# Optimization experiments

Measured on AMD Instinct MI355X. Metric: run time of the kernel, lower is better.

Reference implementation:

```python
import jax, jax.numpy as jnp
import numpy as np

B, S, D, H = 1, 2048, 1024, 16
HD = D // H
THRESHOLD_PCT = 0.95
SPARSITY = 0.9
TOPK = max(1, int(S * (1.0 - SPARSITY)))  # 204


def setup_inputs() -> dict:
    key = jax.random.key(0)
    ks = jax.random.split(key, 6)
    inp = {
        'x': jax.random.normal(ks[0], (B, S, D), dtype=jnp.float32),
        'Wq': jax.random.normal(ks[1], (D, D), dtype=jnp.float32) * 0.02,
        'bq': jnp.zeros((D,), jnp.float32),
        'Wk': jax.random.normal(ks[2], (D, D), dtype=jnp.float32) * 0.02,
        'bk': jnp.zeros((D,), jnp.float32),
        'Wv': jax.random.normal(ks[3], (D, D), dtype=jnp.float32) * 0.02,
        'bv': jnp.zeros((D,), jnp.float32),
        'Wo': jax.random.normal(ks[4], (D, D), dtype=jnp.float32) * 0.02,
        'bo': jnp.zeros((D,), jnp.float32),
    }
    return inp


def _heads(t):  # [B,S,D] -> [B,H,S,HD]
    return t.reshape(B, S, H, HD).transpose(0, 2, 1, 3)


def reference(x, Wq, bq, Wk, bk, Wv, bv, Wo, bo):
    q = _heads(x @ Wq + bq)
    k = _heads(x @ Wk + bk)
    v = _heads(x @ Wv + bv)
    scores = jnp.einsum('bhqd,bhkd->bhqk', q, k) / jnp.sqrt(jnp.float32(HD))

    # --- dynamic threshold mask (per batch,head quantile over all S*S scores) ---
    flat = scores.reshape(B, H, S * S)
    thr = jnp.quantile(flat, THRESHOLD_PCT, axis=-1)[..., None, None]  # [B,H,1,1]
    thresh_mask = scores >= thr
    # fallback: if kept fraction exceeds (1 - sparsity_ratio), use per-row top-k
    cond = jnp.mean(thresh_mask.astype(scores.dtype)) > (1.0 - SPARSITY)
    kth = jax.lax.top_k(scores, TOPK)[0][..., -1:]  # k-th largest per row
    topk_mask = scores >= kth
    mask = jnp.where(cond, topk_mask, thresh_mask)

    masked = jnp.where(mask, scores, -jnp.inf)
    attn = jax.nn.softmax(masked, axis=-1)
    out = jnp.einsum('bhqk,bhkd->bhqd', attn, v)
    out = out.transpose(0, 2, 1, 3).reshape(B, S, D)
    return out @ Wo + bo
```

## Files before the change

kernel.cpp:

```cpp
#include <hip/hip_runtime.h>
#include <math.h>

#define SS 2048
#define DD 1024
#define HH 16
#define CAPC 49152u
#define LCAP 2048

#define K_A 3984587u
#define K_B 3984588u
#define QFRAC 0.85f
#define WSCALE 2048.0f
#define WSCALE_INV (1.0f/2048.0f)
#define ESHIFT 4.0f

typedef _Float16 f16x8 __attribute__((ext_vector_type(8)));
typedef _Float16 f16x4 __attribute__((ext_vector_type(4)));
typedef float    f32x4 __attribute__((ext_vector_type(4)));

__device__ __forceinline__ unsigned sortkey(float f) {
  unsigned b = __float_as_uint(f);
  return (b & 0x80000000u) ? ~b : (b | 0x80000000u);
}
__device__ __forceinline__ float inv_sortkey(unsigned u) {
  unsigned b = (u & 0x80000000u) ? (u ^ 0x80000000u) : ~u;
  return __uint_as_float(b);
}

__global__ __launch_bounds__(256) void split_x(const float* __restrict__ x,
                                               _Float16* __restrict__ xh,
                                               _Float16* __restrict__ xl)
{
  const int i = blockIdx.x * 256 + threadIdx.x;
  float4 v = ((const float4*)x)[i];
  float vv[4] = {v.x, v.y, v.z, v.w};
  f16x4 h, l;
#pragma unroll
  for (int j = 0; j < 4; ++j) {
    _Float16 hh = (_Float16)vv[j];
    h[j] = hh;
    l[j] = (_Float16)(vv[j] - (float)hh);
  }
  ((f16x4*)xh)[i] = h;
  ((f16x4*)xl)[i] = l;
}

__global__ __launch_bounds__(256) void split_wT(const float* __restrict__ Wq,
                                                const float* __restrict__ Wk,
                                                const float* __restrict__ Wv,
                                                const float* __restrict__ Wo,
                                                _Float16* __restrict__ wplanes)
{
  const int z = blockIdx.z;
  const float* W = (z == 0) ? Wq : (z == 1) ? Wk : (z == 2) ? Wv : Wo;
  _Float16* WhT = wplanes + (size_t)(2*z)     * (1024*1024);
  _Float16* WlT = wplanes + (size_t)(2*z + 1) * (1024*1024);
  __shared__ float tile[64][65];
  const int t  = threadIdx.x;
  const int r  = t >> 2;
  const int c0 = (t & 3) * 16;
  const int k0 = blockIdx.y * 64;
  const int n0 = blockIdx.x * 64;
#pragma unroll
  for (int j = 0; j < 4; ++j) {
    float4 v = *(const float4*)&W[(size_t)(k0 + r) * 1024 + n0 + c0 + j*4];
    tile[r][c0+j*4+0] = v.x; tile[r][c0+j*4+1] = v.y;
    tile[r][c0+j*4+2] = v.z; tile[r][c0+j*4+3] = v.w;
  }
  __syncthreads();
  f16x8 h0, h1, l0, l1;
#pragma unroll
  for (int j = 0; j < 8; ++j) {
    float v = tile[c0 + j][r] * WSCALE;
    _Float16 h = (_Float16)v;
    h0[j] = h; l0[j] = (_Float16)(v - (float)h);
  }
#pragma unroll
  for (int j = 0; j < 8; ++j) {
    float v = tile[c0 + 8 + j][r] * WSCALE;
    _Float16 h = (_Float16)v;
    h1[j] = h; l1[j] = (_Float16)(v - (float)h);
  }
  const size_t o = (size_t)(n0 + r) * 1024 + k0 + c0;
  *(f16x8*)&WhT[o]     = h0;
  *(f16x8*)&WhT[o + 8] = h1;
  *(f16x8*)&WlT[o]     = l0;
  *(f16x8*)&WlT[o + 8] = l1;
}

__device__ __forceinline__ void gemm_mfma_body(const _Float16* __restrict__ Ah,
                                               const _Float16* __restrict__ Al,
                                               const _Float16* __restrict__ BhT,
                                               const _Float16* __restrict__ BlT,
                                               const float* __restrict__ bias,
                                               _Float16* __restrict__ Oh,
                                               _Float16* __restrict__ Ol,
                                               float* __restrict__ Of,
                                               int mode, int bm, int bn)
{
  const int wave = threadIdx.x >> 6, lane = threadIdx.x & 63;
  const int wr = wave >> 1, wc = wave & 1;
  const int m0 = bm * 128 + wr * 64;
  const int n0 = bn * 128 + wc * 64;
  const int lr = lane & 15;
  const int ko = lane >> 4;

  f32x4 acc[4][4];
#pragma unroll
  for (int i = 0; i < 4; ++i)
#pragma unroll
    for (int j = 0; j < 4; ++j) acc[i][j] = (f32x4){0.f, 0.f, 0.f, 0.f};

  for (int kk = 0; kk < 32; ++kk) {
    const int kof = kk*32 + ko*8;
    f16x8 aH[4], aL[4], bH[4], bL[4];
#pragma unroll
    for (int i = 0; i < 4; ++i) {
      const size_t aoff = (size_t)(m0 + i*16 + lr) * 1024 + kof;
      aH[i] = *(const f16x8*)(Ah + aoff);
      aL[i] = *(const f16x8*)(Al + aoff);
      const size_t boff = (size_t)(n0 + i*16 + lr) * 1024 + kof;
      bH[i] = *(const f16x8*)(BhT + boff);
      bL[i] = *(const f16x8*)(BlT + boff);
    }
#pragma unroll
    for (int i = 0; i < 4; ++i)
#pragma unroll
      for (int j = 0; j < 4; ++j) {
        acc[i][j] = __builtin_amdgcn_mfma_f32_16x16x32_f16(aL[i], bL[j], acc[i][j], 0, 0, 0);
        acc[i][j] = __builtin_amdgcn_mfma_f32_16x16x32_f16(aH[i], bL[j], acc[i][j], 0, 0, 0);
        acc[i][j] = __builtin_amdgcn_mfma_f32_16x16x32_f16(aL[i], bH[j], acc[i][j], 0, 0, 0);
        acc[i][j] = __builtin_amdgcn_mfma_f32_16x16x32_f16(aH[i], bH[j], acc[i][j], 0, 0, 0);
      }
  }

#pragma unroll
  for (int i = 0; i < 4; ++i) {
#pragma unroll
    for (int j = 0; j < 4; ++j) {
      if (mode == 2) {
        const int col  = n0 + j*16 + lr;
        const int row0 = m0 + i*16 + ko*4;
        f16x4 hv, lv;
#pragma unroll
        for (int r = 0; r < 4; ++r) {
          const float val = acc[i][j][r] * WSCALE_INV + bias[col];
          _Float16 h = (_Float16)val;
          hv[r] = h; lv[r] = (_Float16)(val - (float)h);
        }
        *(f16x4*)&Oh[(size_t)col * 2048 + row0] = hv;
        *(f16x4*)&Ol[(size_t)col * 2048 + row0] = lv;
      } else {
#pragma unroll
        for (int r = 0; r < 4; ++r) {
          const int row = m0 + i*16 + ko*4 + r;
          const int col = n0 + j*16 + lr;
          const float val = acc[i][j][r] * WSCALE_INV + bias[col];
          if (mode == 1) {
            Of[(size_t)row * 1024 + col] = val;
          } else {
            _Float16 h = (_Float16)val;
            Oh[(size_t)row * 1024 + col] = h;
            Ol[(size_t)row * 1024 + col] = (_Float16)(val - (float)h);
          }
        }
      }
    }
  }
}

__global__ __launch_bounds__(256) void gemm_mfma_qkv(const _Float16* __restrict__ xh,
                                                     const _Float16* __restrict__ xl,
                                                     const _Float16* __restrict__ wplanes,
                                                     const float* __restrict__ bq,
                                                     const float* __restrict__ bk,
                                                     const float* __restrict__ bv,
                                                     _Float16* __restrict__ Qh,
                                                     _Float16* __restrict__ Ql,
                                                     _Float16* __restrict__ Kh,
                                                     _Float16* __restrict__ Kl,
                                                     _Float16* __restrict__ VtH,
                                                     _Float16* __restrict__ VtL)
{
  const int z = blockIdx.z;
  const _Float16* BhT = wplanes + (size_t)(2*z)     * (1024*1024);
  const _Float16* BlT = wplanes + (size_t)(2*z + 1) * (1024*1024);
  const float* bias = (z == 0) ? bq : (z == 1) ? bk : bv;
  _Float16* Oh = (z == 0) ? Qh : (z == 1) ? Kh : VtH;
  _Float16* Ol = (z == 0) ? Ql : (z == 1) ? Kl : VtL;
  gemm_mfma_body(xh, xl, BhT, BlT, bias, Oh, Ol, nullptr, (z == 2) ? 2 : 0,
                 blockIdx.y, blockIdx.x);
}

__global__ __launch_bounds__(256) void gemm_mfma_o(const _Float16* __restrict__ ctxh,
                                                   const _Float16* __restrict__ ctxl,
                                                   const _Float16* __restrict__ wplanes,
                                                   const float* __restrict__ bo,
                                                   float* __restrict__ out)
{
  gemm_mfma_body(ctxh, ctxl,
                 wplanes + (size_t)6 * (1024*1024),
                 wplanes + (size_t)7 * (1024*1024),
                 bo, nullptr, nullptr, out, 1, blockIdx.y, blockIdx.x);
}

__global__ __launch_bounds__(512) void scores_hist(const _Float16* __restrict__ Qh,
                                                   const _Float16* __restrict__ Ql,
                                                   const _Float16* __restrict__ Kh,
                                                   const _Float16* __restrict__ Kl,
                                                   unsigned* __restrict__ ghist)
{
  const int bn = blockIdx.x, bm = blockIdx.y, h = blockIdx.z;
  const int wave = threadIdx.x >> 6, lane = threadIdx.x & 63;
  const int wr = wave >> 1, wc = wave & 1;
  const int m0 = bm * 256 + wr * 64;
  const int n0 = bn * 128 + wc * 64;
  const int lr = lane & 15;
  const int ko = lane >> 4;

  __shared__ unsigned lh[16384];
  for (int i = threadIdx.x; i < 16384; i += 512) lh[i] = 0;
  __syncthreads();

  f32x4 acc[4][4];
#pragma unroll
  for (int i = 0; i < 4; ++i)
#pragma unroll
    for (int j = 0; j < 4; ++j) acc[i][j] = (f32x4){0.f, 0.f, 0.f, 0.f};

#pragma unroll
  for (int kk = 0; kk < 2; ++kk) {
    f16x8 aH[4], aL[4], bH[4], bL[4];
#pragma unroll
    for (int i = 0; i < 4; ++i) {
      const size_t aoff = (size_t)(m0 + i*16 + lr) * 1024 + h*64 + kk*32 + ko*8;
      aH[i] = *(const f16x8*)(Qh + aoff);
      aL[i] = *(const f16x8*)(Ql + aoff);
      const size_t boff = (size_t)(n0 + i*16 + lr) * 1024 + h*64 + kk*32 + ko*8;
      bH[i] = *(const f16x8*)(Kh + boff);
      bL[i] = *(const f16x8*)(Kl + boff);
    }
#pragma unroll
    for (int i = 0; i < 4; ++i)
#pragma unroll
      for (int j = 0; j < 4; ++j) {
        acc[i][j] = __builtin_amdgcn_mfma_f32_16x16x32_f16(aL[i], bL[j], acc[i][j], 0, 0, 0);
        acc[i][j] = __builtin_amdgcn_mfma_f32_16x16x32_f16(aH[i], bL[j], acc[i][j], 0, 0, 0);
        acc[i][j] = __builtin_amdgcn_mfma_f32_16x16x32_f16(aL[i], bH[j], acc[i][j], 0, 0, 0);
        acc[i][j] = __builtin_amdgcn_mfma_f32_16x16x32_f16(aH[i], bH[j], acc[i][j], 0, 0, 0);
      }
  }

#pragma unroll
  for (int i = 0; i < 4; ++i)
#pragma unroll
    for (int j = 0; j < 4; ++j)
#pragma unroll
      for (int r = 0; r < 4; ++r) {
        const float val = acc[i][j][r] * 0.125f;
        atomicAdd(&lh[sortkey(val) >> 18], 1u);
      }
  __syncthreads();
  unsigned* __restrict__ gh = ghist + (size_t)h * 16384;
  for (int i = threadIdx.x; i < 16384; i += 512) {
    const unsigned c = lh[i];
    if (c) atomicAdd(&gh[i], c);
  }
}

__global__ __launch_bounds__(256) void init14(unsigned* __restrict__ ghist,
                                              unsigned* __restrict__ ccnt)
{
  int i = blockIdx.x * 256 + threadIdx.x;
  for (; i < HH * 16384; i += gridDim.x * 256) ghist[i] = 0;
  if (blockIdx.x == 0 && threadIdx.x < HH) ccnt[threadIdx.x] = 0;
}

__global__ __launch_bounds__(256) void scan14(const unsigned* __restrict__ ghist,
                                              unsigned* __restrict__ state)
{
  const int hh = blockIdx.x;
  const int t = threadIdx.x;
  __shared__ unsigned part[256];
  __shared__ unsigned out[4];
  const unsigned* __restrict__ hb = ghist + (size_t)hh * 16384;
  unsigned s = 0;
  for (int j = 0; j < 64; ++j) s += hb[t*64 + j];
  part[t] = s;
  __syncthreads();
  if (t == 0) {
    unsigned run = 0;
    for (int i = 0; i < 256; ++i) { unsigned tmp = part[i]; part[i] = run; run += tmp; }
  }
  __syncthreads();
  const unsigned cum0 = part[t];
  if (K_A >= cum0 && K_A < cum0 + s) {
    unsigned c2 = cum0;
    for (int j = 0; j < 64; ++j) {
      const unsigned c = hb[t*64 + j];
      if (K_A < c2 + c) {
        const unsigned binA = t*64 + j;
        const unsigned residA = K_A - c2;
        unsigned binB, residB;
        if (residA + 1 < c) { binB = binA; residB = residA + 1; }
        else {
          unsigned bb = binA + 1;
          while (bb < 16384 && hb[bb] == 0) ++bb;
          if (bb >= 16384) bb = 16383;
          binB = bb; residB = 0;
        }
        out[0] = binA; out[1] = residA; out[2] = binB; out[3] = residB;
        break;
      }
      c2 += c;
    }
  }
  __syncthreads();
  if (t < 4) state[hh*4 + t] = out[t];
}

__global__ __launch_bounds__(512) void compact_recompute(const _Float16* __restrict__ Qh,
                                                         const _Float16* __restrict__ Ql,
                                                         const _Float16* __restrict__ Kh,
                                                         const _Float16* __restrict__ Kl,
                                                         const unsigned* __restrict__ state,
                                                         unsigned* __restrict__ cand,
                                                         unsigned* __restrict__ ccnt)
{
  const int bn = blockIdx.x, bm = blockIdx.y, h = blockIdx.z;
  const int wave = threadIdx.x >> 6, lane = threadIdx.x & 63;
  const int wr = wave >> 1, wc = wave & 1;
  const int m0 = bm * 256 + wr * 64;
  const int n0 = bn * 128 + wc * 64;
  const int lr = lane & 15;
  const int ko = lane >> 4;

  __shared__ unsigned lbuf[LCAP];
  __shared__ unsigned lcnt, gbase;
  if (threadIdx.x == 0) lcnt = 0;
  __syncthreads();
  const unsigned binA = state[h*4+0];
  const unsigned binB = state[h*4+2];
  unsigned* __restrict__ mycand = cand + (size_t)h * CAPC;

  f32x4 acc[4][4];
#pragma unroll
  for (int i = 0; i < 4; ++i)
#pragma unroll
    for (int j = 0; j < 4; ++j) acc[i][j] = (f32x4){0.f, 0.f, 0.f, 0.f};

#pragma unroll
  for (int kk = 0; kk < 2; ++kk) {
    f16x8 aH[4], aL[4], bH[4], bL[4];
#pragma unroll
    for (int i = 0; i < 4; ++i) {
      const size_t aoff = (size_t)(m0 + i*16 + lr) * 1024 + h*64 + kk*32 + ko*8;
      aH[i] = *(const f16x8*)(Qh + aoff);
      aL[i] = *(const f16x8*)(Ql + aoff);
      const size_t boff = (size_t)(n0 + i*16 + lr) * 1024 + h*64 + kk*32 + ko*8;
      bH[i] = *(const f16x8*)(Kh + boff);
      bL[i] = *(const f16x8*)(Kl + boff);
    }
#pragma unroll
    for (int i = 0; i < 4; ++i)
#pragma unroll
      for (int j = 0; j < 4; ++j) {
        acc[i][j] = __builtin_amdgcn_mfma_f32_16x16x32_f16(aL[i], bL[j], acc[i][j], 0, 0, 0);
        acc[i][j] = __builtin_amdgcn_mfma_f32_16x16x32_f16(aH[i], bL[j], acc[i][j], 0, 0, 0);
        acc[i][j] = __builtin_amdgcn_mfma_f32_16x16x32_f16(aL[i], bH[j], acc[i][j], 0, 0, 0);
        acc[i][j] = __builtin_amdgcn_mfma_f32_16x16x32_f16(aH[i], bH[j], acc[i][j], 0, 0, 0);
      }
  }

#pragma unroll
  for (int i = 0; i < 4; ++i)
#pragma unroll
    for (int j = 0; j < 4; ++j)
#pragma unroll
      for (int r = 0; r < 4; ++r) {
        const float val = acc[i][j][r] * 0.125f;
        const unsigned u = sortkey(val);
        const unsigned bin = u >> 18;
        if (bin == binA || bin == binB) {
          unsigned id = atomicAdd(&lcnt, 1u);
          if (id < LCAP) lbuf[id] = u;
          else { unsigned g = atomicAdd(&ccnt[h], 1u); if (g < CAPC) mycand[g] = u; }
        }
      }
  __syncthreads();
  const unsigned n = (lcnt < LCAP) ? lcnt : LCAP;
  if (threadIdx.x == 0) gbase = n ? atomicAdd(&ccnt[h], n) : 0u;
  __syncthreads();
  const unsigned gb = gbase;
  for (unsigned i = threadIdx.x; i < n; i += 512)
    if (gb + i < CAPC) mycand[gb + i] = lbuf[i];
}

__global__ __launch_bounds__(256) void final_select_list(const unsigned* __restrict__ cand,
                                                         const unsigned* __restrict__ ccnt,
                                                         const unsigned* __restrict__ state,
                                                         float* __restrict__ thr)
{
  const int hh = blockIdx.x;
  const int t = threadIdx.x;
  __shared__ unsigned hist[256];
  __shared__ unsigned digitS, kresS;
  __shared__ float valS[2];
  unsigned n = ccnt[hh]; if (n > CAPC) n = CAPC;
  const unsigned* __restrict__ list = cand + (size_t)hh * CAPC;
  for (int tgt = 0; tgt < 2; ++tgt) {
    unsigned pfx = state[hh*4 + tgt*2];
    unsigned k   = state[hh*4 + tgt*2 + 1];
    for (int r = 0; r < 3; ++r) {
      const int s = (r == 0) ? 10 : (r == 1) ? 2 : 0;
      const int w = (r == 2) ? 2 : 8;
      const unsigned nb = 1u << w;
      hist[t] = 0;
      __syncthreads();
      for (unsigned i = t; i < n; i += 256) {
        const unsigned u = list[i];
        if ((u >> (s + w)) == pfx) atomicAdd(&hist[(u >> s) & (nb - 1)], 1u);
      }
      __syncthreads();
      if (t == 0) {
        unsigned cum = 0, b = 0;
        for (; b < nb; ++b) { const unsigned c = hist[b]; if (cum + c > k) break; cum += c; }
        if (b == nb) b = nb - 1;
        digitS = b; kresS = k - cum;
      }
      __syncthreads();
      pfx = (pfx << w) | digitS;
      k = kresS;
    }
    if (t == 0) valS[tgt] = inv_sortkey(pfx);
    __syncthreads();
  }
  if (t == 0) thr[hh] = valS[0] + QFRAC * (valS[1] - valS[0]);
}

__global__ __launch_bounds__(256) void flash_pv(const _Float16* __restrict__ Qh,
                                                const _Float16* __restrict__ Ql,
                                                const _Float16* __restrict__ Kh,
                                                const _Float16* __restrict__ Kl,
                                                const _Float16* __restrict__ VtH,
                                                const _Float16* __restrict__ VtL,
                                                const float* __restrict__ thrArr,
                                                _Float16* __restrict__ ctxh,
                                                _Float16* __restrict__ ctxl)
{
  const int bm = blockIdx.x;
  const int h  = blockIdx.y;
  const int wave = threadIdx.x >> 6, lane = threadIdx.x & 63;
  const int lr = lane & 15;
  const int ko = lane >> 4;
  const int m0 = bm * 64;
  const float thr = thrArr[h];

  __shared__ _Float16 Plds[64][136];
  __shared__ float rsLDS[64][4];

  f16x8 qH[4][2], qL[4][2];
#pragma unroll
  for (int i = 0; i < 4; ++i)
#pragma unroll
    for (int kk = 0; kk < 2; ++kk) {
      const size_t aoff = (size_t)(m0 + i*16 + lr) * 1024 + h*64 + kk*32 + ko*8;
      qH[i][kk] = *(const f16x8*)(Qh + aoff);
      qL[i][kk] = *(const f16x8*)(Ql + aoff);
    }

  f32x4 oacc[4];
#pragma unroll
  for (int i = 0; i < 4; ++i) oacc[i] = (f32x4){0.f, 0.f, 0.f, 0.f};
  float rs[4][4];
#pragma unroll
  for (int i = 0; i < 4; ++i)
#pragma unroll
    for (int r = 0; r < 4; ++r) rs[i][r] = 0.f;

  const int d0 = wave * 16;

  for (int kt = 0; kt < 16; ++kt) {
    const int n0 = kt*128 + wave*32;
    f32x4 sacc[4][2];
#pragma unroll
    for (int i = 0; i < 4; ++i)
#pragma unroll
      for (int j = 0; j < 2; ++j) sacc[i][j] = (f32x4){0.f, 0.f, 0.f, 0.f};

#pragma unroll
    for (int kk = 0; kk < 2; ++kk) {
      f16x8 bH[2], bL[2];
#pragma unroll
      for (int j = 0; j < 2; ++j) {
        const size_t boff = (size_t)(n0 + j*16 + lr) * 1024 + h*64 + kk*32 + ko*8;
        bH[j] = *(const f16x8*)(Kh + boff);
        bL[j] = *(const f16x8*)(Kl + boff);
      }
#pragma unroll
      for (int i = 0; i < 4; ++i)
#pragma unroll
        for (int j = 0; j < 2; ++j) {
          sacc[i][j] = __builtin_amdgcn_mfma_f32_16x16x32_f16(qL[i][kk], bL[j], sacc[i][j], 0, 0, 0);
          sacc[i][j] = __builtin_amdgcn_mfma_f32_16x16x32_f16(qH[i][kk], bL[j], sacc[i][j], 0, 0, 0);
          sacc[i][j] = __builtin_amdgcn_mfma_f32_16x16x32_f16(qL[i][kk], bH[j], sacc[i][j], 0, 0, 0);
          sacc[i][j] = __builtin_amdgcn_mfma_f32_16x16x32_f16(qH[i][kk], bH[j], sacc[i][j], 0, 0, 0);
        }
    }

#pragma unroll
    for (int i = 0; i < 4; ++i)
#pragma unroll
      for (int j = 0; j < 2; ++j)
#pragma unroll
        for (int r = 0; r < 4; ++r) {
          const float val = sacc[i][j][r] * 0.125f;
          const float p = (val >= thr) ? __expf(val - thr - ESHIFT) : 0.f;
          rs[i][r] += p;
          Plds[i*16 + ko*4 + r][wave*32 + j*16 + lr] = (_Float16)p;
        }
    __syncthreads();

#pragma unroll
    for (int kk2 = 0; kk2 < 4; ++kk2) {
      f16x8 pa[4];
#pragma unroll
      for (int i = 0; i < 4; ++i)
        pa[i] = *(const f16x8*)&Plds[i*16 + lr][kk2*32 + ko*8];
      const size_t vo = (size_t)(h*64 + d0 + lr) * 2048 + kt*128 + kk2*32 + ko*8;
      const f16x8 vH = *(const f16x8*)(VtH + vo);
      const f16x8 vL = *(const f16x8*)(VtL + vo);
#pragma unroll
      for (int i = 0; i < 4; ++i) {
        oacc[i] = __builtin_amdgcn_mfma_f32_16x16x32_f16(pa[i], vL, oacc[i], 0, 0, 0);
        oacc[i] = __builtin_amdgcn_mfma_f32_16x16x32_f16(pa[i], vH, oacc[i], 0, 0, 0);
      }
    }
    __syncthreads();
  }

#pragma unroll
  for (int i = 0; i < 4; ++i)
#pragma unroll
    for (int r = 0; r < 4; ++r) {
      float v = rs[i][r];
      v += __shfl_xor(v, 1); v += __shfl_xor(v, 2);
      v += __shfl_xor(v, 4); v += __shfl_xor(v, 8);
      rs[i][r] = v;
    }
  if (lr == 0) {
#pragma unroll
    for (int i = 0; i < 4; ++i)
#pragma unroll
      for (int r = 0; r < 4; ++r)
        rsLDS[i*16 + ko*4 + r][wave] = rs[i][r];
  }
  __syncthreads();

#pragma unroll
  for (int i = 0; i < 4; ++i)
#pragma unroll
    for (int r = 0; r < 4; ++r) {
      const int lrow = i*16 + ko*4 + r;
      const float tot = rsLDS[lrow][0] + rsLDS[lrow][1] + rsLDS[lrow][2] + rsLDS[lrow][3];
      const float val = oacc[i][r] / tot;
      const size_t oidx = (size_t)(m0 + lrow) * 1024 + h*64 + d0 + lr;
      _Float16 hv = (_Float16)val;
      ctxh[oidx] = hv;
      ctxl[oidx] = (_Float16)(val - (float)hv);
    }
}

extern "C" void kernel_launch(void* const* d_in, const int* in_sizes, int n_in,
                              void* d_out, int out_size, void* d_ws, size_t ws_size,
                              hipStream_t stream)
{
  const float* x  = (const float*)d_in[0];
  const float* Wq = (const float*)d_in[1];
  const float* bq = (const float*)d_in[2];
  const float* Wk = (const float*)d_in[3];
  const float* bk = (const float*)d_in[4];
  const float* Wv = (const float*)d_in[5];
  const float* bv = (const float*)d_in[6];
  const float* Wo = (const float*)d_in[7];
  const float* bo = (const float*)d_in[8];
  float* out = (float*)d_out;
  char*  ws  = (char*)d_ws;

  const size_t MB = 1u << 20;
  _Float16* xh      = (_Float16*)(ws + 0*MB);
  _Float16* xl      = (_Float16*)(ws + 4*MB);
  _Float16* wplanes = (_Float16*)(ws + 8*MB);
  _Float16* Qh      = (_Float16*)(ws + 24*MB);
  _Float16* Ql      = (_Float16*)(ws + 28*MB);
  _Float16* Kh      = (_Float16*)(ws + 32*MB);
  _Float16* Kl      = (_Float16*)(ws + 36*MB);
  _Float16* VtH     = (_Float16*)(ws + 40*MB);
  _Float16* VtL     = (_Float16*)(ws + 44*MB);
  _Float16* ctxh    = (_Float16*)(ws + 48*MB);
  _Float16* ctxl    = (_Float16*)(ws + 52*MB);
  const size_t base = 56*MB;
  unsigned* state = (unsigned*)(ws + base);
  float*    thr   = (float*)(ws + base + 4096);
  unsigned* ccnt  = (unsigned*)(ws + base + 8192);
  unsigned* ghist = (unsigned*)(ws + base + 16384);
  unsigned* cand  = (unsigned*)(ws + base + 16384 + 1048576);

  split_x<<<2048, 256, 0, stream>>>(x, xh, xl);
  split_wT<<<dim3(16, 16, 4), 256, 0, stream>>>(Wq, Wk, Wv, Wo, wplanes);
  gemm_mfma_qkv<<<dim3(8, 16, 3), 256, 0, stream>>>(xh, xl, wplanes, bq, bk, bv,
                                                    Qh, Ql, Kh, Kl, VtH, VtL);

  init14<<<256, 256, 0, stream>>>(ghist, ccnt);
  scores_hist<<<dim3(16, 8, HH), 512, 0, stream>>>(Qh, Ql, Kh, Kl, ghist);
  scan14<<<HH, 256, 0, stream>>>(ghist, state);
  compact_recompute<<<dim3(16, 8, HH), 512, 0, stream>>>(Qh, Ql, Kh, Kl, state, cand, ccnt);
  final_select_list<<<HH, 256, 0, stream>>>(cand, ccnt, state, thr);
  flash_pv<<<dim3(32, HH), 256, 0, stream>>>(Qh, Ql, Kh, Kl, VtH, VtL, thr, ctxh, ctxl);

  gemm_mfma_o<<<dim3(8, 16), 256, 0, stream>>>(ctxh, ctxl, wplanes, bo, out);
}
```

Before: 601.1 us.

## Split GEMM tiles across 8 waves with register prefetch, halve flash_pv rows

The QKV and output GEMMs now run 512-thread blocks, with each of 8 waves owning a 64x32 sub-tile instead of 64x64. The K-loop loads the next k-slice of A and B fragments into registers while the MFMAs for the current slice run. flash_pv handles 32 query rows per block instead of 64 and launches twice as many blocks. The aim is more waves in flight and latency hiding on the global loads, at the cost of more redundant K/V loads in flash_pv and more A-fragment reloads across waves in the GEMMs.

```diff
diff --git a/kernel.cpp b/kernel.cpp
--- a/kernel.cpp
+++ b/kernel.cpp
@@ -99,45 +99,73 @@
                                                int mode, int bm, int bn)
 {
   const int wave = threadIdx.x >> 6, lane = threadIdx.x & 63;
-  const int wr = wave >> 1, wc = wave & 1;
+  const int wr = wave >> 2, wc = wave & 3;
   const int m0 = bm * 128 + wr * 64;
-  const int n0 = bn * 128 + wc * 64;
+  const int n0 = bn * 128 + wc * 32;
   const int lr = lane & 15;
   const int ko = lane >> 4;
 
-  f32x4 acc[4][4];
+  f32x4 acc[4][2];
 #pragma unroll
   for (int i = 0; i < 4; ++i)
 #pragma unroll
-    for (int j = 0; j < 4; ++j) acc[i][j] = (f32x4){0.f, 0.f, 0.f, 0.f};
-
-  for (int kk = 0; kk < 32; ++kk) {
-    const int kof = kk*32 + ko*8;
-    f16x8 aH[4], aL[4], bH[4], bL[4];
+    for (int j = 0; j < 2; ++j) acc[i][j] = (f32x4){0.f, 0.f, 0.f, 0.f};
+
+  f16x8 aH[4], aL[4], bH[2], bL[2];
+  {
+    const int kof = ko*8;
 #pragma unroll
     for (int i = 0; i < 4; ++i) {
       const size_t aoff = (size_t)(m0 + i*16 + lr) * 1024 + kof;
       aH[i] = *(const f16x8*)(Ah + aoff);
       aL[i] = *(const f16x8*)(Al + aoff);
-      const size_t boff = (size_t)(n0 + i*16 + lr) * 1024 + kof;
-      bH[i] = *(const f16x8*)(BhT + boff);
-      bL[i] = *(const f16x8*)(BlT + boff);
+    }
+#pragma unroll
+    for (int j = 0; j < 2; ++j) {
+      const size_t boff = (size_t)(n0 + j*16 + lr) * 1024 + kof;
+      bH[j] = *(const f16x8*)(BhT + boff);
+      bL[j] = *(const f16x8*)(BlT + boff);
+    }
+  }
+
+  for (int kk = 0; kk < 32; ++kk) {
+    f16x8 nAH[4], nAL[4], nBH[2], nBL[2];
+    if (kk < 31) {
+      const int kof = (kk+1)*32 + ko*8;
+#pragma unroll
+      for (int i = 0; i < 4; ++i) {
+        const size_t aoff = (size_t)(m0 + i*16 + lr) * 1024 + kof;
+        nAH[i] = *(const f16x8*)(Ah + aoff);
+        nAL[i] = *(const f16x8*)(Al + aoff);
+      }
+#pragma unroll
+      for (int j = 0; j < 2; ++j) {
+        const size_t boff = (size_t)(n0 + j*16 + lr) * 1024 + kof;
+        nBH[j] = *(const f16x8*)(BhT + boff);
+        nBL[j] = *(const f16x8*)(BlT + boff);
+      }
     }
 #pragma unroll
     for (int i = 0; i < 4; ++i)
 #pragma unroll
-      for (int j = 0; j < 4; ++j) {
+      for (int j = 0; j < 2; ++j) {
         acc[i][j] = __builtin_amdgcn_mfma_f32_16x16x32_f16(aL[i], bL[j], acc[i][j], 0, 0, 0);
         acc[i][j] = __builtin_amdgcn_mfma_f32_16x16x32_f16(aH[i], bL[j], acc[i][j], 0, 0, 0);
         acc[i][j] = __builtin_amdgcn_mfma_f32_16x16x32_f16(aL[i], bH[j], acc[i][j], 0, 0, 0);
         acc[i][j] = __builtin_amdgcn_mfma_f32_16x16x32_f16(aH[i], bH[j], acc[i][j], 0, 0, 0);
       }
+    if (kk < 31) {
+#pragma unroll
+      for (int i = 0; i < 4; ++i) { aH[i] = nAH[i]; aL[i] = nAL[i]; }
+#pragma unroll
+      for (int j = 0; j < 2; ++j) { bH[j] = nBH[j]; bL[j] = nBL[j]; }
+    }
   }
 
 #pragma unroll
   for (int i = 0; i < 4; ++i) {
 #pragma unroll
-    for (int j = 0; j < 4; ++j) {
+    for (int j = 0; j < 2; ++j) {
       if (mode == 2) {
         const int col  = n0 + j*16 + lr;
         const int row0 = m0 + i*16 + ko*4;
@@ -169,7 +197,7 @@
   }
 }
 
-__global__ __launch_bounds__(256) void gemm_mfma_qkv(const _Float16* __restrict__ xh,
+__global__ __launch_bounds__(512) void gemm_mfma_qkv(const _Float16* __restrict__ xh,
                                                      const _Float16* __restrict__ xl,
                                                      const _Float16* __restrict__ wplanes,
                                                      const float* __restrict__ bq,
@@ -192,7 +220,7 @@
                  blockIdx.y, blockIdx.x);
 }
 
-__global__ __launch_bounds__(256) void gemm_mfma_o(const _Float16* __restrict__ ctxh,
+__global__ __launch_bounds__(512) void gemm_mfma_o(const _Float16* __restrict__ ctxh,
                                                    const _Float16* __restrict__ ctxl,
                                                    const _Float16* __restrict__ wplanes,
                                                    const float* __restrict__ bo,
@@ -453,15 +481,15 @@
   const int wave = threadIdx.x >> 6, lane = threadIdx.x & 63;
   const int lr = lane & 15;
   const int ko = lane >> 4;
-  const int m0 = bm * 64;
+  const int m0 = bm * 32;
   const float thr = thrArr[h];
 
-  __shared__ _Float16 Plds[64][136];
-  __shared__ float rsLDS[64][4];
-
-  f16x8 qH[4][2], qL[4][2];
-#pragma unroll
-  for (int i = 0; i < 4; ++i)
+  __shared__ _Float16 Plds[32][136];
+  __shared__ float rsLDS[32][4];
+
+  f16x8 qH[2][2], qL[2][2];
+#pragma unroll
+  for (int i = 0; i < 2; ++i)
 #pragma unroll
     for (int kk = 0; kk < 2; ++kk) {
       const size_t aoff = (size_t)(m0 + i*16 + lr) * 1024 + h*64 + kk*32 + ko*8;
@@ -469,12 +497,12 @@
       qL[i][kk] = *(const f16x8*)(Ql + aoff);
     }
 
-  f32x4 oacc[4];
-#pragma unroll
-  for (int i = 0; i < 4; ++i) oacc[i] = (f32x4){0.f, 0.f, 0.f, 0.f};
-  float rs[4][4];
-#pragma unroll
-  for (int i = 0; i < 4; ++i)
+  f32x4 oacc[2];
+#pragma unroll
+  for (int i = 0; i < 2; ++i) oacc[i] = (f32x4){0.f, 0.f, 0.f, 0.f};
+  float rs[2][4];
+#pragma unroll
+  for (int i = 0; i < 2; ++i)
 #pragma unroll
     for (int r = 0; r < 4; ++r) rs[i][r] = 0.f;
 
@@ -482,9 +510,9 @@
 
   for (int kt = 0; kt < 16; ++kt) {
     const int n0 = kt*128 + wave*32;
-    f32x4 sacc[4][2];
-#pragma unroll
-    for (int i = 0; i < 4; ++i)
+    f32x4 sacc[2][2];
+#pragma unroll
+    for (int i = 0; i < 2; ++i)
 #pragma unroll
       for (int j = 0; j < 2; ++j) sacc[i][j] = (f32x4){0.f, 0.f, 0.f, 0.f};
 
@@ -498,7 +526,7 @@
         bL[j] = *(const f16x8*)(Kl + boff);
       }
 #pragma unroll
-      for (int i = 0; i < 4; ++i)
+      for (int i = 0; i < 2; ++i)
 #pragma unroll
         for (int j = 0; j < 2; ++j) {
           sacc[i][j] = __builtin_amdgcn_mfma_f32_16x16x32_f16(qL[i][kk], bL[j], sacc[i][j], 0, 0, 0);
@@ -509,7 +537,7 @@
     }
 
 #pragma unroll
-    for (int i = 0; i < 4; ++i)
+    for (int i = 0; i < 2; ++i)
 #pragma unroll
       for (int j = 0; j < 2; ++j)
 #pragma unroll
@@ -523,15 +551,15 @@
 
 #pragma unroll
     for (int kk2 = 0; kk2 < 4; ++kk2) {
-      f16x8 pa[4];
-#pragma unroll
-      for (int i = 0; i < 4; ++i)
+      f16x8 pa[2];
+#pragma unroll
+      for (int i = 0; i < 2; ++i)
         pa[i] = *(const f16x8*)&Plds[i*16 + lr][kk2*32 + ko*8];
       const size_t vo = (size_t)(h*64 + d0 + lr) * 2048 + kt*128 + kk2*32 + ko*8;
       const f16x8 vH = *(const f16x8*)(VtH + vo);
       const f16x8 vL = *(const f16x8*)(VtL + vo);
 #pragma unroll
-      for (int i = 0; i < 4; ++i) {
+      for (int i = 0; i < 2; ++i) {
         oacc[i] = __builtin_amdgcn_mfma_f32_16x16x32_f16(pa[i], vL, oacc[i], 0, 0, 0);
         oacc[i] = __builtin_amdgcn_mfma_f32_16x16x32_f16(pa[i], vH, oacc[i], 0, 0, 0);
       }
@@ -540,7 +568,7 @@
   }
 
 #pragma unroll
-  for (int i = 0; i < 4; ++i)
+  for (int i = 0; i < 2; ++i)
 #pragma unroll
     for (int r = 0; r < 4; ++r) {
       float v = rs[i][r];
@@ -550,7 +578,7 @@
     }
   if (lr == 0) {
 #pragma unroll
-    for (int i = 0; i < 4; ++i)
+    for (int i = 0; i < 2; ++i)
 #pragma unroll
       for (int r = 0; r < 4; ++r)
         rsLDS[i*16 + ko*4 + r][wave] = rs[i][r];
@@ -558,7 +586,7 @@
   __syncthreads();
 
 #pragma unroll
-  for (int i = 0; i < 4; ++i)
+  for (int i = 0; i < 2; ++i)
 #pragma unroll
     for (int r = 0; r < 4; ++r) {
       const int lrow = i*16 + ko*4 + r;
@@ -608,7 +636,7 @@
 
   split_x<<<2048, 256, 0, stream>>>(x, xh, xl);
   split_wT<<<dim3(16, 16, 4), 256, 0, stream>>>(Wq, Wk, Wv, Wo, wplanes);
-  gemm_mfma_qkv<<<dim3(8, 16, 3), 256, 0, stream>>>(xh, xl, wplanes, bq, bk, bv,
+  gemm_mfma_qkv<<<dim3(8, 16, 3), 512, 0, stream>>>(xh, xl, wplanes, bq, bk, bv,
                                                     Qh, Ql, Kh, Kl, VtH, VtL);
 
   init14<<<256, 256, 0, stream>>>(ghist, ccnt);
@@ -616,7 +644,7 @@
   scan14<<<HH, 256, 0, stream>>>(ghist, state);
   compact_recompute<<<dim3(16, 8, HH), 512, 0, stream>>>(Qh, Ql, Kh, Kl, state, cand, ccnt);
   final_select_list<<<HH, 256, 0, stream>>>(cand, ccnt, state, thr);
-  flash_pv<<<dim3(32, HH), 256, 0, stream>>>(Qh, Ql, Kh, Kl, VtH, VtL, thr, ctxh, ctxl);
-
-  gemm_mfma_o<<<dim3(8, 16), 256, 0, stream>>>(ctxh, ctxl, wplanes, bo, out);
-}
+  flash_pv<<<dim3(64, HH), 256, 0, stream>>>(Qh, Ql, Kh, Kl, VtH, VtL, thr, ctxh, ctxl);
+
+  gemm_mfma_o<<<dim3(8, 16), 512, 0, stream>>>(ctxh, ctxl, wplanes, bo, out);
+}
```

After: 719.9 us. 1.2x slower.

## Split-K the QKV, output GEMMs and flash PV with separate combine kernels

Applied to the files above, without the earlier changes.

Splits the K dimension of the QKV and output projection GEMMs, and the key range of the flash PV kernel, into two halves. This doubles the number of blocks so more of the GPU's compute units stay busy. The partial fp32 results go to workspace buffers and are then reduced by new combine kernels, which also apply bias, row normalization, fp16 hi/lo splitting and the V transpose. The cost is extra global memory traffic for the fp32 partials plus several additional kernel launches. The flash split drops the per-row max rescaling between halves, which is only safe if both halves use a fixed shift.

```diff
diff --git a/kernel.cpp b/kernel.cpp
--- a/kernel.cpp
+++ b/kernel.cpp
@@ -13,6 +13,7 @@
 #define WSCALE 2048.0f
 #define WSCALE_INV (1.0f/2048.0f)
 #define ESHIFT 4.0f
+#define PLANE 2097152
 
 typedef _Float16 f16x8 __attribute__((ext_vector_type(8)));
 typedef _Float16 f16x4 __attribute__((ext_vector_type(4)));
@@ -88,15 +89,12 @@
   *(f16x8*)&WlT[o + 8] = l1;
 }
 
-__device__ __forceinline__ void gemm_mfma_body(const _Float16* __restrict__ Ah,
+__device__ __forceinline__ void gemm_mfma_part(const _Float16* __restrict__ Ah,
                                                const _Float16* __restrict__ Al,
                                                const _Float16* __restrict__ BhT,
                                                const _Float16* __restrict__ BlT,
-                                               const float* __restrict__ bias,
-                                               _Float16* __restrict__ Oh,
-                                               _Float16* __restrict__ Ol,
-                                               float* __restrict__ Of,
-                                               int mode, int bm, int bn)
+                                               float* __restrict__ pout,
+                                               int bm, int bn, int kh)
 {
   const int wave = threadIdx.x >> 6, lane = threadIdx.x & 63;
   const int wr = wave >> 1, wc = wave & 1;
@@ -111,7 +109,7 @@
 #pragma unroll
     for (int j = 0; j < 4; ++j) acc[i][j] = (f32x4){0.f, 0.f, 0.f, 0.f};
 
-  for (int kk = 0; kk < 32; ++kk) {
+  for (int kk = kh*16; kk < kh*16 + 16; ++kk) {
     const int kof = kk*32 + ko*8;
     f16x8 aH[4], aL[4], bH[4], bL[4];
 #pragma unroll
@@ -135,73 +133,163 @@
   }
 
 #pragma unroll
-  for (int i = 0; i < 4; ++i) {
-#pragma unroll
-    for (int j = 0; j < 4; ++j) {
-      if (mode == 2) {
-        const int col  = n0 + j*16 + lr;
-        const int row0 = m0 + i*16 + ko*4;
-        f16x4 hv, lv;
-#pragma unroll
-        for (int r = 0; r < 4; ++r) {
-          const float val = acc[i][j][r] * WSCALE_INV + bias[col];
-          _Float16 h = (_Float16)val;
-          hv[r] = h; lv[r] = (_Float16)(val - (float)h);
-        }
-        *(f16x4*)&Oh[(size_t)col * 2048 + row0] = hv;
-        *(f16x4*)&Ol[(size_t)col * 2048 + row0] = lv;
-      } else {
-#pragma unroll
-        for (int r = 0; r < 4; ++r) {
-          const int row = m0 + i*16 + ko*4 + r;
-          const int col = n0 + j*16 + lr;
-          const float val = acc[i][j][r] * WSCALE_INV + bias[col];
-          if (mode == 1) {
-            Of[(size_t)row * 1024 + col] = val;
-          } else {
-            _Float16 h = (_Float16)val;
-            Oh[(size_t)row * 1024 + col] = h;
-            Ol[(size_t)row * 1024 + col] = (_Float16)(val - (float)h);
-          }
-        }
-      }
-    }
-  }
-}
-
-__global__ __launch_bounds__(256) void gemm_mfma_qkv(const _Float16* __restrict__ xh,
+  for (int i = 0; i < 4; ++i)
+#pragma unroll
+    for (int j = 0; j < 4; ++j)
+#pragma unroll
+      for (int r = 0; r < 4; ++r) {
+        const int row = m0 + i*16 + ko*4 + r;
+        const int col = n0 + j*16 + lr;
+        pout[(size_t)row * 1024 + col] = acc[i][j][r];
+      }
+}
+
+__global__ __launch_bounds__(256) void gemm_qkv_part(const _Float16* __restrict__ xh,
                                                      const _Float16* __restrict__ xl,
                                                      const _Float16* __restrict__ wplanes,
-                                                     const float* __restrict__ bq,
-                                                     const float* __restrict__ bk,
-                                                     const float* __restrict__ bv,
-                                                     _Float16* __restrict__ Qh,
-                                                     _Float16* __restrict__ Ql,
-                                                     _Float16* __restrict__ Kh,
-                                                     _Float16* __restrict__ Kl,
-                                                     _Float16* __restrict__ VtH,
-                                                     _Float16* __restrict__ VtL)
+                                                     float* __restrict__ pbuf)
 {
   const int z = blockIdx.z;
-  const _Float16* BhT = wplanes + (size_t)(2*z)     * (1024*1024);
-  const _Float16* BlT = wplanes + (size_t)(2*z + 1) * (1024*1024);
-  const float* bias = (z == 0) ? bq : (z == 1) ? bk : bv;
-  _Float16* Oh = (z == 0) ? Qh : (z == 1) ? Kh : VtH;
-  _Float16* Ol = (z == 0) ? Ql : (z == 1) ? Kl : VtL;
-  gemm_mfma_body(xh, xl, BhT, BlT, bias, Oh, Ol, nullptr, (z == 2) ? 2 : 0,
-                 blockIdx.y, blockIdx.x);
-}
-
-__global__ __launch_bounds__(256) void gemm_mfma_o(const _Float16* __restrict__ ctxh,
+  const int g = z >> 1, kh = z & 1;
+  const _Float16* BhT = wplanes + (size_t)(2*g)     * (1024*1024);
+  const _Float16* BlT = wplanes + (size_t)(2*g + 1) * (1024*1024);
+  gemm_mfma_part(xh, xl, BhT, BlT, pbuf + (size_t)z * PLANE,
+                 blockIdx.y, blockIdx.x, kh);
+}
+
+__global__ __launch_bounds__(256) void gemm_o_part(const _Float16* __restrict__ ctxh,
                                                    const _Float16* __restrict__ ctxl,
                                                    const _Float16* __restrict__ wplanes,
-                                                   const float* __restrict__ bo,
-                                                   float* __restrict__ out)
-{
-  gemm_mfma_body(ctxh, ctxl,
+                                                   float* __restrict__ pO)
+{
+  const int kh = blockIdx.z;
+  gemm_mfma_part(ctxh, ctxl,
                  wplanes + (size_t)6 * (1024*1024),
                  wplanes + (size_t)7 * (1024*1024),
-                 bo, nullptr, nullptr, out, 1, blockIdx.y, blockIdx.x);
+                 pO + (size_t)kh * PLANE, blockIdx.y, blockIdx.x, kh);
+}
+
+__global__ __launch_bounds__(256) void combine_qk(const float* __restrict__ pbuf,
+                                                  const float* __restrict__ bq,
+                                                  const float* __restrict__ bk,
+                                                  _Float16* __restrict__ Qh,
+                                                  _Float16* __restrict__ Ql,
+                                                  _Float16* __restrict__ Kh,
+                                                  _Float16* __restrict__ Kl)
+{
+  const int which = blockIdx.y;
+  const float* p0 = pbuf + (size_t)(which*2)     * PLANE;
+  const float* p1 = pbuf + (size_t)(which*2 + 1) * PLANE;
+  const float* bias = which ? bk : bq;
+  _Float16* Oh = which ? Kh : Qh;
+  _Float16* Ol = which ? Kl : Ql;
+  const int i = blockIdx.x * 256 + threadIdx.x;
+  const int coloff = (i & 255) * 4;
+  float4 a = ((const float4*)p0)[i];
+  float4 b = ((const float4*)p1)[i];
+  float av[4] = {a.x, a.y, a.z, a.w};
+  float bv[4] = {b.x, b.y, b.z, b.w};
+  f16x4 h, l;
+#pragma unroll
+  for (int j = 0; j < 4; ++j) {
+    const float val = (av[j] + bv[j]) * WSCALE_INV + bias[coloff + j];
+    _Float16 hh = (_Float16)val;
+    h[j] = hh;
+    l[j] = (_Float16)(val - (float)hh);
+  }
+  ((f16x4*)Oh)[i] = h;
+  ((f16x4*)Ol)[i] = l;
+}
+
+__global__ __launch_bounds__(256) void combine_vT(const float* __restrict__ pbuf,
+                                                  const float* __restrict__ bv,
+                                                  _Float16* __restrict__ VtH,
+                                                  _Float16* __restrict__ VtL)
+{
+  const float* p0 = pbuf + (size_t)4 * PLANE;
+  const float* p1 = pbuf + (size_t)5 * PLANE;
+  __shared__ float tile[64][65];
+  const int t  = threadIdx.x;
+  const int d0 = blockIdx.x * 64;
+  const int m0 = blockIdx.y * 64;
+  {
+    const int r  = t >> 2;
+    const int c0 = (t & 3) * 16;
+#pragma unroll
+    for (int j = 0; j < 4; ++j) {
+      const size_t o = (size_t)(m0 + r) * 1024 + d0 + c0 + j*4;
+      float4 a = *(const float4*)(p0 + o);
+      float4 b = *(const float4*)(p1 + o);
+      tile[r][c0+j*4+0] = (a.x + b.x) * WSCALE_INV + bv[d0 + c0 + j*4 + 0];
+      tile[r][c0+j*4+1] = (a.y + b.y) * WSCALE_INV + bv[d0 + c0 + j*4 + 1];
+      tile[r][c0+j*4+2] = (a.z + b.z) * WSCALE_INV + bv[d0 + c0 + j*4 + 2];
+      tile[r][c0+j*4+3] = (a.w + b.w) * WSCALE_INV + bv[d0 + c0 + j*4 + 3];
+    }
+  }
+  __syncthreads();
+  {
+    const int d  = t >> 2;
+    const int rg = (t & 3) * 16;
+#pragma unroll
+    for (int j = 0; j < 4; ++j) {
+      f16x4 hv, lv;
+#pragma unroll
+      for (int r = 0; r < 4; ++r) {
+        const float val = tile[rg + j*4 + r][d];
+        _Float16 h = (_Float16)val;
+        hv[r] = h; lv[r] = (_Float16)(val - (float)h);
+      }
+      const size_t o = (size_t)(d0 + d) * 2048 + m0 + rg + j*4;
+      *(f16x4*)&VtH[o] = hv;
+      *(f16x4*)&VtL[o] = lv;
+    }
+  }
+}
+
+__global__ __launch_bounds__(256) void combine_o(const float* __restrict__ pO,
+                                                 const float* __restrict__ bo,
+                                                 float* __restrict__ out)
+{
+  const float* p0 = pO;
+  const float* p1 = pO + (size_t)1 * PLANE;
+  const int i = blockIdx.x * 256 + threadIdx.x;
+  const int coloff = (i & 255) * 4;
+  float4 a = ((const float4*)p0)[i];
+  float4 b = ((const float4*)p1)[i];
+  float4 o;
+  o.x = (a.x + b.x) * WSCALE_INV + bo[coloff + 0];
+  o.y = (a.y + b.y) * WSCALE_INV + bo[coloff + 1];
+  o.z = (a.z + b.z) * WSCALE_INV + bo[coloff + 2];
+  o.w = (a.w + b.w) * WSCALE_INV + bo[coloff + 3];
+  ((float4*)out)[i] = o;
+}
+
+__global__ __launch_bounds__(256) void combine_ctx(const float* __restrict__ pctx,
+                                                   const float* __restrict__ prs,
+                                                   _Float16* __restrict__ ctxh,
+                                                   _Float16* __restrict__ ctxl)
+{
+  const float* p0 = pctx;
+  const float* p1 = pctx + (size_t)1 * PLANE;
+  const int i = blockIdx.x * 256 + threadIdx.x;
+  const int row = i >> 8;
+  const int cd  = (i & 255) * 4;
+  const int h   = cd >> 6;
+  const float rs = prs[h*2048 + row] + prs[32768 + h*2048 + row];
+  float4 a = ((const float4*)p0)[i];
+  float4 b = ((const float4*)p1)[i];
+  float av[4] = {a.x, a.y, a.z, a.w};
+  float bv[4] = {b.x, b.y, b.z, b.w};
+  f16x4 hh, ll;
+#pragma unroll
+  for (int j = 0; j < 4; ++j) {
+    const float val = (av[j] + bv[j]) / rs;
+    _Float16 hv = (_Float16)val;
+    hh[j] = hv;
+    ll[j] = (_Float16)(val - (float)hv);
+  }
+  ((f16x4*)ctxh)[i] = hh;
+  ((f16x4*)ctxl)[i] = ll;
 }
 
 __global__ __launch_bounds__(512) void scores_hist(const _Float16* __restrict__ Qh,
@@ -438,18 +526,19 @@
   if (t == 0) thr[hh] = valS[0] + QFRAC * (valS[1] - valS[0]);
 }
 
-__global__ __launch_bounds__(256) void flash_pv(const _Float16* __restrict__ Qh,
-                                                const _Float16* __restrict__ Ql,
-                                                const _Float16* __restrict__ Kh,
-                                                const _Float16* __restrict__ Kl,
-                                                const _Float16* __restrict__ VtH,
-                                                const _Float16* __restrict__ VtL,
-                                                const float* __restrict__ thrArr,
-                                                _Float16* __restrict__ ctxh,
-                                                _Float16* __restrict__ ctxl)
+__global__ __launch_bounds__(256) void flash_pv_sk(const _Float16* __restrict__ Qh,
+                                                   const _Float16* __restrict__ Ql,
+                                                   const _Float16* __restrict__ Kh,
+                                                   const _Float16* __restrict__ Kl,
+                                                   const _Float16* __restrict__ VtH,
+                                                   const _Float16* __restrict__ VtL,
+                                                   const float* __restrict__ thrArr,
+                                                   float* __restrict__ pctx,
+                                                   float* __restrict__ prs)
 {
   const int bm = blockIdx.x;
   const int h  = blockIdx.y;
+  const int half = blockIdx.z;
   const int wave = threadIdx.x >> 6, lane = threadIdx.x & 63;
   const int lr = lane & 15;
   const int ko = lane >> 4;
@@ -480,7 +569,7 @@
 
   const int d0 = wave * 16;
 
-  for (int kt = 0; kt < 16; ++kt) {
+  for (int kt = half*8; kt < half*8 + 8; ++kt) {
     const int n0 = kt*128 + wave*32;
     f32x4 sacc[4][2];
 #pragma unroll
@@ -557,17 +646,24 @@
   }
   __syncthreads();
 
+  if (wave == 0 && lr == 0) {
+#pragma unroll
+    for (int i = 0; i < 4; ++i)
+#pragma unroll
+      for (int r = 0; r < 4; ++r) {
+        const int lrow = i*16 + ko*4 + r;
+        prs[half*32768 + h*2048 + m0 + lrow] =
+            rsLDS[lrow][0] + rsLDS[lrow][1] + rsLDS[lrow][2] + rsLDS[lrow][3];
+      }
+  }
+
+  float* __restrict__ pc = pctx + (size_t)half * PLANE;
 #pragma unroll
   for (int i = 0; i < 4; ++i)
 #pragma unroll
     for (int r = 0; r < 4; ++r) {
       const int lrow = i*16 + ko*4 + r;
-      const float tot = rsLDS[lrow][0] + rsLDS[lrow][1] + rsLDS[lrow][2] + rsLDS[lrow][3];
-      const float val = oacc[i][r] / tot;
-      const size_t oidx = (size_t)(m0 + lrow) * 1024 + h*64 + d0 + lr;
-      _Float16 hv = (_Float16)val;
-      ctxh[oidx] = hv;
-      ctxl[oidx] = (_Float16)(val - (float)hv);
+      pc[(size_t)(m0 + lrow) * 1024 + h*64 + d0 + lr] = oacc[i][r];
     }
 }
 
@@ -605,18 +701,25 @@
   unsigned* ccnt  = (unsigned*)(ws + base + 8192);
   unsigned* ghist = (unsigned*)(ws + base + 16384);
   unsigned* cand  = (unsigned*)(ws + base + 16384 + 1048576);
+  float*    prs   = (float*)(ws + 61*MB);
+  float*    pbuf  = (float*)(ws + 64*MB);
+  float*    pctx  = pbuf;
+  float*    pO    = pbuf + (size_t)2 * PLANE;
 
   split_x<<<2048, 256, 0, stream>>>(x, xh, xl);
   split_wT<<<dim3(16, 16, 4), 256, 0, stream>>>(Wq, Wk, Wv, Wo, wplanes);
-  gemm_mfma_qkv<<<dim3(8, 16, 3), 256, 0, stream>>>(xh, xl, wplanes, bq, bk, bv,
-                                                    Qh, Ql, Kh, Kl, VtH, VtL);
+  gemm_qkv_part<<<dim3(8, 16, 6), 256, 0, stream>>>(xh, xl, wplanes, pbuf);
+  combine_qk<<<dim3(2048, 2), 256, 0, stream>>>(pbuf, bq, bk, Qh, Ql, Kh, Kl);
+  combine_vT<<<dim3(16, 32), 256, 0, stream>>>(pbuf, bv, VtH, VtL);
 
   init14<<<256, 256, 0, stream>>>(ghist, ccnt);
   scores_hist<<<dim3(16, 8, HH), 512, 0, stream>>>(Qh, Ql, Kh, Kl, ghist);
   scan14<<<HH, 256, 0, stream>>>(ghist, state);
   compact_recompute<<<dim3(16, 8, HH), 512, 0, stream>>>(Qh, Ql, Kh, Kl, state, cand, ccnt);
   final_select_list<<<HH, 256, 0, stream>>>(cand, ccnt, state, thr);
-  flash_pv<<<dim3(32, HH), 256, 0, stream>>>(Qh, Ql, Kh, Kl, VtH, VtL, thr, ctxh, ctxl);
-
-  gemm_mfma_o<<<dim3(8, 16), 256, 0, stream>>>(ctxh, ctxl, wplanes, bo, out);
-}
+  flash_pv_sk<<<dim3(32, HH, 2), 256, 0, stream>>>(Qh, Ql, Kh, Kl, VtH, VtL, thr, pctx, prs);
+  combine_ctx<<<2048, 256, 0, stream>>>(pctx, prs, ctxh, ctxl);
+
+  gemm_o_part<<<dim3(8, 16, 2), 256, 0, stream>>>(ctxh, ctxl, wplanes, pO);
+  combine_o<<<2048, 256, 0, stream>>>(pO, bo, out);
+}
```

After: 578.7 us. -3.7%, faster.
